# Kernel tuning notes

Measured on AMD Instinct MI355X. Metric: run time of the kernel, lower is better.

The kernel has to match this reference:

```python
import jax, jax.numpy as jnp
import numpy as np

NUM_EMBEDDINGS = 512
EMBEDDING_DIM = 64
COMMITMENT_COST = 0.25


def setup_inputs() -> dict:
    key = jax.random.key(0)
    k_in, k_cb = jax.random.split(key)
    inputs = jax.random.normal(k_in, (32, EMBEDDING_DIM, 64, 64), dtype=jnp.float32)
    # nn.Embedding weight initialized uniform(-1/K, 1/K)
    codebook = jax.random.uniform(
        k_cb, (NUM_EMBEDDINGS, EMBEDDING_DIM), dtype=jnp.float32,
        minval=-1.0 / NUM_EMBEDDINGS, maxval=1.0 / NUM_EMBEDDINGS)
    return {"inputs": inputs, "codebook": codebook}


def reference(inputs, codebook):
    N, D, H, W = inputs.shape
    # [N, H, W, D] -> [N*H*W, D]
    flat = jnp.transpose(inputs, (0, 2, 3, 1)).reshape(-1, D)
    # Squared euclidean distances (argmin identical to cdist's euclidean argmin)
    d2 = (jnp.sum(flat * flat, axis=1, keepdims=True)
          - 2.0 * flat @ codebook.T
          + jnp.sum(codebook * codebook, axis=1))  # [N*H*W, K]
    encoding_index = jnp.argmin(d2, axis=1)  # [N*H*W]
    quantized = codebook[encoding_index]      # gather [N*H*W, D]
    quantized = quantized.reshape(N, H, W, D).transpose(0, 3, 1, 2)  # [N, D, H, W]
    e_latent_loss = jnp.mean((jax.lax.stop_gradient(quantized) - inputs) ** 2)
    q_latent_loss = jnp.mean((quantized - jax.lax.stop_gradient(inputs)) ** 2)
    c_loss = q_latent_loss + COMMITMENT_COST * e_latent_loss
    # straight-through estimator
    quantized_st = inputs + jax.lax.stop_gradient(quantized - inputs)
    return (c_loss, quantized_st)
```

## Files before the change

### kernel.cpp

```cpp
#include <hip/hip_runtime.h>

#define DIM 64
#define HW 4096
#define NELEM 8388608.0f
#define NBLK 2048

typedef __attribute__((ext_vector_type(8))) short short8;
typedef __attribute__((ext_vector_type(4))) float f32x4;

__device__ __forceinline__ unsigned short f2bf(float f) {
  unsigned int u = __builtin_bit_cast(unsigned int, f);
  u += 0x7fffu + ((u >> 16) & 1u);
  return (unsigned short)(u >> 16);
}

__device__ __forceinline__ float wave_sum(float v) {
  #pragma unroll
  for (int off = 32; off >= 1; off >>= 1) v += __shfl_xor(v, off);
  return v;
}


__global__ void vq_prep(const float* __restrict__ CB,
                        unsigned short* __restrict__ aFg,
                        float* __restrict__ cn) {
  const int t = threadIdx.x;
  const int s = blockIdx.x * 512 + t;
  const int chunk = s >> 7, ks = (s >> 6) & 1, ls = s & 63;
  const int code = chunk * 16 + (ls & 15);
  const int d0 = ks * 32 + (ls >> 4) * 8;
  const float* cp = CB + code * DIM + d0;
  float4 u0 = *(const float4*)cp;
  float4 u1 = *(const float4*)(cp + 4);
  short8 p;
  p[0]=(short)f2bf(-2.f*u0.x); p[1]=(short)f2bf(-2.f*u0.y);
  p[2]=(short)f2bf(-2.f*u0.z); p[3]=(short)f2bf(-2.f*u0.w);
  p[4]=(short)f2bf(-2.f*u1.x); p[5]=(short)f2bf(-2.f*u1.y);
  p[6]=(short)f2bf(-2.f*u1.z); p[7]=(short)f2bf(-2.f*u1.w);
  *(short8*)&aFg[s * 8] = p;
  if (blockIdx.x == 0) {
    const float* c2 = CB + t * DIM;
    float sn = 0.f;
    #pragma unroll
    for (int i = 0; i < 16; ++i) {
      float4 u = *(const float4*)(c2 + i * 4);
      sn += u.x*u.x + u.y*u.y + u.z*u.z + u.w*u.w;
    }
    cn[t] = sn;
  }
}

__global__ __launch_bounds__(256, 4)
void vq_main(const float* __restrict__ X, const float* __restrict__ CB,
             const unsigned short* __restrict__ aFg,
             const float* __restrict__ cng,
             float* __restrict__ out,
             float* __restrict__ pA, float* __restrict__ pB) {
  __shared__ __align__(16) unsigned short XF[8 * 64 * 8];
  __shared__ float mW[4][64];
  __shared__ float red[8];

  const int t   = threadIdx.x;
  const int bid = blockIdx.x;
  const int L   = ((bid & 7) << 8) | (bid >> 3);
  const int n   = L >> 6;
  const int hw0 = (L & 63) << 6;
  const int wv  = t >> 6, lane = t & 63;
  const int g   = lane >> 4, lcol = lane & 15;

  const float* Xg = X + n * (DIM * HW) + hw0;

  const int db8 = t >> 5;
  const int cp  = t & 31;
  const int kss = db8 >> 2, gs = db8 & 3;
  float2 v[8];
  #pragma unroll
  for (int j = 0; j < 8; ++j)
    v[j] = *(const float2*)(Xg + (db8 * 8 + j) * HW + cp * 2);
  float sx2 = 0.f;
  #pragma unroll
  for (int j = 0; j < 8; ++j)
    sx2 += v[j].x * v[j].x + v[j].y * v[j].y;
  #pragma unroll
  for (int ci = 0; ci < 2; ++ci) {
    const int c = cp * 2 + ci;
    const int slot = ((c >> 4) * 2 + kss) * 64 + gs * 16 + (c & 15);
    const int swz  = slot ^ ((slot >> 3) & 7);
    short8 w;
    #pragma unroll
    for (int j = 0; j < 8; ++j)
      w[j] = (short)f2bf(ci ? v[j].y : v[j].x);
    *(short8*)&XF[swz * 8] = w;
  }
  __syncthreads();

  const int s64  = g * 16 + lcol;
  const int swzl = s64 ^ ((s64 >> 3) & 7);
  short8 bfrag[4][2];
  #pragma unroll
  for (int cb = 0; cb < 4; ++cb) {
    #pragma unroll
    for (int ks = 0; ks < 2; ++ks)
      bfrag[cb][ks] = *(const short8*)&XF[((cb * 2 + ks) * 64 + swzl) * 8];
  }

  float m1[4];
  #pragma unroll
  for (int cb = 0; cb < 4; ++cb) m1[cb] = 3.0e38f;

  const int chunk0 = wv * 8;
  #pragma unroll 4
  for (int i = 0; i < 8; ++i) {
    const int chunk = chunk0 + i;
    const short8 a0 = *(const short8*)&aFg[((chunk*2 + 0) * 64 + lane) * 8];
    const short8 a1 = *(const short8*)&aFg[((chunk*2 + 1) * 64 + lane) * 8];
    const int codebase = chunk * 16 + g * 4;
    const f32x4 cn = *(const f32x4*)&cng[codebase];
    #pragma unroll
    for (int cb = 0; cb < 4; ++cb) {
      f32x4 acc = cn;
      acc = __builtin_amdgcn_mfma_f32_16x16x32_bf16(a0, bfrag[cb][0], acc, 0, 0, 0);
      acc = __builtin_amdgcn_mfma_f32_16x16x32_bf16(a1, bfrag[cb][1], acc, 0, 0, 0);
      #pragma unroll
      for (int r = 0; r < 4; ++r) {
        unsigned int vb = __builtin_bit_cast(unsigned int, acc[r]);
        vb = (vb & 0xFFFFFE00u) | ((unsigned)(codebase + r) & 0x1FFu);
        m1[cb] = fminf(m1[cb], __builtin_bit_cast(float, vb));
      }
    }
  }

  #pragma unroll
  for (int cb = 0; cb < 4; ++cb) {
    m1[cb] = fminf(m1[cb], __shfl_xor(m1[cb], 16));
    m1[cb] = fminf(m1[cb], __shfl_xor(m1[cb], 32));
    if (g == 0) mW[wv][cb * 16 + lcol] = m1[cb];
  }
  __syncthreads();

  const float p = fminf(fminf(mW[0][lane], mW[1][lane]),
                        fminf(mW[2][lane], mW[3][lane]));
  const unsigned int b = __builtin_bit_cast(unsigned int, p);
  const int k = (int)(b & 511u);
  const float minval = __builtin_bit_cast(float, b & 0xFFFFFE00u);

  const float* cq = CB + k * DIM + wv * 16;
  float* op = out + 1 + n * (DIM * HW) + hw0 + lane;
  #pragma unroll
  for (int i = 0; i < 4; ++i) {
    float4 u = *(const float4*)(cq + i * 4);
    op[(wv*16 + i*4 + 0) * HW] = u.x;
    op[(wv*16 + i*4 + 1) * HW] = u.y;
    op[(wv*16 + i*4 + 2) * HW] = u.z;
    op[(wv*16 + i*4 + 3) * HW] = u.w;
  }

  float w1 = wave_sum(sx2);
  if (lane == 0) red[wv] = w1;
  if (wv == 0) {
    float w2 = wave_sum(minval);
    if (lane == 0) red[4] = w2;
  }
  __syncthreads();
  if (t == 0) {
    pA[bid] = red[0] + red[1] + red[2] + red[3];
    pB[bid] = red[4];
  }
}

__global__ void vq_fin(const float* __restrict__ pA,
                       const float* __restrict__ pB,
                       float* __restrict__ out) {
  const int t = threadIdx.x;
  float4 a = *(const float4*)&pA[t * 4];
  float4 c = *(const float4*)&pB[t * 4];
  float v = a.x + a.y + a.z + a.w + c.x + c.y + c.z + c.w;
  v = wave_sum(v);
  __shared__ float r[8];
  if ((t & 63) == 0) r[t >> 6] = v;
  __syncthreads();
  if (t == 0) {
    float s = 0.f;
    #pragma unroll
    for (int i = 0; i < 8; ++i) s += r[i];
    out[0] = 1.25f * s * (1.0f / NELEM);
  }
}

extern "C" void kernel_launch(void* const* d_in, const int* in_sizes, int n_in,
                              void* d_out, int out_size, void* d_ws, size_t ws_size,
                              hipStream_t stream) {
  const float* X  = (const float*)d_in[0];
  const float* CB = (const float*)d_in[1];
  float* out = (float*)d_out;
  char* ws = (char*)d_ws;
  unsigned short* aFg = (unsigned short*)ws;
  float* cn = (float*)(ws + 65536);
  float* pA = (float*)(ws + 67584);
  float* pB = (float*)(ws + 75776);
  (void)in_sizes; (void)n_in; (void)out_size; (void)ws_size;

  vq_prep<<<8, 512, 0, stream>>>(CB, aFg, cn);
  vq_main<<<NBLK, 256, 0, stream>>>(X, CB, aFg, cn, out, pA, pB);
  vq_fin<<<1, 512, 0, stream>>>(pA, pB, out);
}
```

Before: 35.41 us.

## Process 128 pixels per block to amortize codebook fragment loads

Each block now handles 128 spatial positions instead of 64, so the grid halves to 1024 blocks. Each codebook A-fragment loaded from global memory now feeds twice as many MFMAs, and the LDS staging and min-reduction buffers double to match. Input loads and output stores switch to nontemporal hints to avoid polluting cache with streaming data. The per-thread register footprint grows (16 B-fragments, 8 running minima), which can lower occupancy, and there are fewer blocks to fill the GPU.

Measured after the change: 34.25 us. -3.3%, faster.

```diff
diff --git a/kernel.cpp b/kernel.cpp
--- a/kernel.cpp
+++ b/kernel.cpp
@@ -3,10 +3,11 @@
 #define DIM 64
 #define HW 4096
 #define NELEM 8388608.0f
-#define NBLK 2048
+#define NBLK 1024
 
 typedef __attribute__((ext_vector_type(8))) short short8;
 typedef __attribute__((ext_vector_type(4))) float f32x4;
+typedef __attribute__((ext_vector_type(2))) float f32x2;
 
 __device__ __forceinline__ unsigned short f2bf(float f) {
   unsigned int u = __builtin_bit_cast(unsigned int, f);
@@ -56,15 +57,15 @@
              const float* __restrict__ cng,
              float* __restrict__ out,
              float* __restrict__ pA, float* __restrict__ pB) {
-  __shared__ __align__(16) unsigned short XF[8 * 64 * 8];
-  __shared__ float mW[4][64];
+  __shared__ __align__(16) unsigned short XF[16 * 64 * 8];
+  __shared__ float mW[4][128];
   __shared__ float red[8];
 
   const int t   = threadIdx.x;
   const int bid = blockIdx.x;
-  const int L   = ((bid & 7) << 8) | (bid >> 3);
-  const int n   = L >> 6;
-  const int hw0 = (L & 63) << 6;
+  const int L   = ((bid & 7) << 7) | (bid >> 3);
+  const int n   = L >> 5;
+  const int hw0 = (L & 31) << 7;
   const int wv  = t >> 6, lane = t & 63;
   const int g   = lane >> 4, lcol = lane & 15;
 
@@ -73,43 +74,53 @@
   const int db8 = t >> 5;
   const int cp  = t & 31;
   const int kss = db8 >> 2, gs = db8 & 3;
-  float2 v[8];
-  #pragma unroll
-  for (int j = 0; j < 8; ++j)
-    v[j] = *(const float2*)(Xg + (db8 * 8 + j) * HW + cp * 2);
+  f32x2 v[2][8];
+  #pragma unroll
+  for (int h = 0; h < 2; ++h)
+    #pragma unroll
+    for (int j = 0; j < 8; ++j)
+      v[h][j] = __builtin_nontemporal_load(
+          (const f32x2*)(Xg + (db8 * 8 + j) * HW + h * 64 + cp * 2));
   float sx2 = 0.f;
   #pragma unroll
-  for (int j = 0; j < 8; ++j)
-    sx2 += v[j].x * v[j].x + v[j].y * v[j].y;
-  #pragma unroll
-  for (int ci = 0; ci < 2; ++ci) {
-    const int c = cp * 2 + ci;
-    const int slot = ((c >> 4) * 2 + kss) * 64 + gs * 16 + (c & 15);
-    const int swz  = slot ^ ((slot >> 3) & 7);
-    short8 w;
+  for (int h = 0; h < 2; ++h)
     #pragma unroll
     for (int j = 0; j < 8; ++j)
-      w[j] = (short)f2bf(ci ? v[j].y : v[j].x);
-    *(short8*)&XF[swz * 8] = w;
-  }
-  __syncthreads();
-
-  const int s64  = g * 16 + lcol;
-  const int swzl = s64 ^ ((s64 >> 3) & 7);
-  short8 bfrag[4][2];
-  #pragma unroll
-  for (int cb = 0; cb < 4; ++cb) {
-    #pragma unroll
-    for (int ks = 0; ks < 2; ++ks)
-      bfrag[cb][ks] = *(const short8*)&XF[((cb * 2 + ks) * 64 + swzl) * 8];
-  }
-
-  float m1[4];
-  #pragma unroll
-  for (int cb = 0; cb < 4; ++cb) m1[cb] = 3.0e38f;
+      sx2 += v[h][j].x * v[h][j].x + v[h][j].y * v[h][j].y;
+  #pragma unroll
+  for (int h = 0; h < 2; ++h) {
+    #pragma unroll
+    for (int ci = 0; ci < 2; ++ci) {
+      const int cl   = cp * 2 + ci;
+      const int cb   = h * 4 + (cl >> 4);
+      const int slot = (cb * 2 + kss) * 64 + gs * 16 + (cl & 15);
+      const int swz  = slot ^ ((slot >> 3) & 7);
+      short8 w;
+      #pragma unroll
+      for (int j = 0; j < 8; ++j)
+        w[j] = (short)f2bf(ci ? v[h][j].y : v[h][j].x);
+      *(short8*)&XF[swz * 8] = w;
+    }
+  }
+  __syncthreads();
+
+  const int swzl = lane ^ ((lane >> 3) & 7);
+  short8 bfrag[2][4][2];
+  #pragma unroll
+  for (int h = 0; h < 2; ++h)
+    #pragma unroll
+    for (int cb2 = 0; cb2 < 4; ++cb2)
+      #pragma unroll
+      for (int ks = 0; ks < 2; ++ks)
+        bfrag[h][cb2][ks] =
+            *(const short8*)&XF[(((h * 4 + cb2) * 2 + ks) * 64 + swzl) * 8];
+
+  float m1[8];
+  #pragma unroll
+  for (int cb = 0; cb < 8; ++cb) m1[cb] = 3.0e38f;
 
   const int chunk0 = wv * 8;
-  #pragma unroll 4
+  #pragma unroll 2
   for (int i = 0; i < 8; ++i) {
     const int chunk = chunk0 + i;
     const short8 a0 = *(const short8*)&aFg[((chunk*2 + 0) * 64 + lane) * 8];
@@ -117,48 +128,56 @@
     const int codebase = chunk * 16 + g * 4;
     const f32x4 cn = *(const f32x4*)&cng[codebase];
     #pragma unroll
-    for (int cb = 0; cb < 4; ++cb) {
-      f32x4 acc = cn;
-      acc = __builtin_amdgcn_mfma_f32_16x16x32_bf16(a0, bfrag[cb][0], acc, 0, 0, 0);
-      acc = __builtin_amdgcn_mfma_f32_16x16x32_bf16(a1, bfrag[cb][1], acc, 0, 0, 0);
+    for (int h = 0; h < 2; ++h) {
       #pragma unroll
-      for (int r = 0; r < 4; ++r) {
-        unsigned int vb = __builtin_bit_cast(unsigned int, acc[r]);
-        vb = (vb & 0xFFFFFE00u) | ((unsigned)(codebase + r) & 0x1FFu);
-        m1[cb] = fminf(m1[cb], __builtin_bit_cast(float, vb));
+      for (int cb2 = 0; cb2 < 4; ++cb2) {
+        f32x4 acc = cn;
+        acc = __builtin_amdgcn_mfma_f32_16x16x32_bf16(a0, bfrag[h][cb2][0], acc, 0, 0, 0);
+        acc = __builtin_amdgcn_mfma_f32_16x16x32_bf16(a1, bfrag[h][cb2][1], acc, 0, 0, 0);
+        #pragma unroll
+        for (int r = 0; r < 4; ++r) {
+          unsigned int vb = __builtin_bit_cast(unsigned int, acc[r]);
+          vb = (vb & 0xFFFFFE00u) | ((unsigned)(codebase + r) & 0x1FFu);
+          m1[h * 4 + cb2] = fminf(m1[h * 4 + cb2], __builtin_bit_cast(float, vb));
+        }
       }
     }
   }
 
   #pragma unroll
-  for (int cb = 0; cb < 4; ++cb) {
+  for (int cb = 0; cb < 8; ++cb) {
     m1[cb] = fminf(m1[cb], __shfl_xor(m1[cb], 16));
     m1[cb] = fminf(m1[cb], __shfl_xor(m1[cb], 32));
     if (g == 0) mW[wv][cb * 16 + lcol] = m1[cb];
   }
   __syncthreads();
 
-  const float p = fminf(fminf(mW[0][lane], mW[1][lane]),
-                        fminf(mW[2][lane], mW[3][lane]));
-  const unsigned int b = __builtin_bit_cast(unsigned int, p);
-  const int k = (int)(b & 511u);
-  const float minval = __builtin_bit_cast(float, b & 0xFFFFFE00u);
-
-  const float* cq = CB + k * DIM + wv * 16;
-  float* op = out + 1 + n * (DIM * HW) + hw0 + lane;
-  #pragma unroll
-  for (int i = 0; i < 4; ++i) {
-    float4 u = *(const float4*)(cq + i * 4);
-    op[(wv*16 + i*4 + 0) * HW] = u.x;
-    op[(wv*16 + i*4 + 1) * HW] = u.y;
-    op[(wv*16 + i*4 + 2) * HW] = u.z;
-    op[(wv*16 + i*4 + 3) * HW] = u.w;
+  float msum = 0.f;
+  #pragma unroll
+  for (int h = 0; h < 2; ++h) {
+    const int c = h * 64 + lane;
+    const float p = fminf(fminf(mW[0][c], mW[1][c]),
+                          fminf(mW[2][c], mW[3][c]));
+    const unsigned int b = __builtin_bit_cast(unsigned int, p);
+    const int k = (int)(b & 511u);
+    msum += __builtin_bit_cast(float, b & 0xFFFFFE00u);
+
+    const float* cq = CB + k * DIM + wv * 16;
+    float* op = out + 1 + n * (DIM * HW) + hw0 + c;
+    #pragma unroll
+    for (int i = 0; i < 4; ++i) {
+      float4 u = *(const float4*)(cq + i * 4);
+      __builtin_nontemporal_store(u.x, &op[(wv*16 + i*4 + 0) * HW]);
+      __builtin_nontemporal_store(u.y, &op[(wv*16 + i*4 + 1) * HW]);
+      __builtin_nontemporal_store(u.z, &op[(wv*16 + i*4 + 2) * HW]);
+      __builtin_nontemporal_store(u.w, &op[(wv*16 + i*4 + 3) * HW]);
+    }
   }
 
   float w1 = wave_sum(sx2);
   if (lane == 0) red[wv] = w1;
   if (wv == 0) {
-    float w2 = wave_sum(minval);
+    float w2 = wave_sum(msum);
     if (lane == 0) red[4] = w2;
   }
   __syncthreads();
@@ -172,9 +191,9 @@
                        const float* __restrict__ pB,
                        float* __restrict__ out) {
   const int t = threadIdx.x;
-  float4 a = *(const float4*)&pA[t * 4];
-  float4 c = *(const float4*)&pB[t * 4];
-  float v = a.x + a.y + a.z + a.w + c.x + c.y + c.z + c.w;
+  f32x2 a = *(const f32x2*)&pA[t * 2];
+  f32x2 c = *(const f32x2*)&pB[t * 2];
+  float v = a.x + a.y + c.x + c.y;
   v = wave_sum(v);
   __shared__ float r[8];
   if ((t & 63) == 0) r[t >> 6] = v;
```
